# Kernel tuning notes

Measured on AMD Instinct MI355X. Metric: run time of the kernel, lower is better.

The kernel has to match this reference:

```python
import jax, jax.numpy as jnp
from jax import lax
import numpy as np

VOCAB = 50000
EMBED = 300
H = 128
NUM_CLASS = 2
B, L = 4, 512


def _lstm(x, Wih, Whh, b):
    # x: (B, L, D) -> hidden sequence (B, L, H); PyTorch gate order i,f,g,o
    Bn = x.shape[0]
    h0 = jnp.zeros((Bn, H), dtype=x.dtype)
    c0 = jnp.zeros((Bn, H), dtype=x.dtype)

    def step(carry, xt):
        h, c = carry
        g = xt @ Wih + h @ Whh + b  # (B, 4H)
        i, f, gg, o = jnp.split(g, 4, axis=-1)
        i = jax.nn.sigmoid(i)
        f = jax.nn.sigmoid(f)
        gg = jnp.tanh(gg)
        o = jax.nn.sigmoid(o)
        c = f * c + i * gg
        h = o * jnp.tanh(c)
        return (h, c), h

    _, hs = lax.scan(step, (h0, c0), jnp.swapaxes(x, 0, 1))
    return jnp.swapaxes(hs, 0, 1)


def setup_inputs() -> dict:
    key = jax.random.key(0)
    ks = jax.random.split(key, 12)
    s = lambda fan_in: 1.0 / np.sqrt(fan_in)
    inp = {
        "question_content": jax.random.randint(ks[0], (B, L), 0, VOCAB, dtype=jnp.int32),
        "answer_content": jax.random.randint(ks[1], (B, L), 0, VOCAB, dtype=jnp.int32),
        "embed_table": jax.random.normal(ks[2], (VOCAB, EMBED), dtype=jnp.float32) * 0.1,
        "W_ih": jax.random.uniform(ks[3], (EMBED, 4 * H), jnp.float32, -s(H), s(H)),
        "W_hh": jax.random.uniform(ks[4], (H, 4 * H), jnp.float32, -s(H), s(H)),
        "b_lstm": jax.random.uniform(ks[5], (4 * H,), jnp.float32, -s(H), s(H)),
        "Wa": jax.random.uniform(ks[6], (2 * H, H), jnp.float32, -s(2 * H), s(2 * H)),
        "ba": jnp.zeros((H,), jnp.float32),
        "Wq": jax.random.uniform(ks[7], (2 * H, 1), jnp.float32, -s(2 * H), s(2 * H)),
        "bq": jnp.zeros((1,), jnp.float32),
        "Wans": jax.random.uniform(ks[8], (2 * H, 1), jnp.float32, -s(2 * H), s(2 * H)),
        "bans": jnp.zeros((1,), jnp.float32),
        "Wlast": jax.random.uniform(ks[9], (2 * H, NUM_CLASS), jnp.float32, -s(2 * H), s(2 * H)),
        "blast": jnp.zeros((NUM_CLASS,), jnp.float32),
    }
    return inp


def reference(question_content, answer_content, embed_table, W_ih, W_hh, b_lstm,
              Wa, ba, Wq, bq, Wans, bans, Wlast, blast):
    q_emb = embed_table[question_content]  # (B, Lq, EMBED)
    a_emb = embed_table[answer_content]    # (B, La, EMBED)
    q_lstm = _lstm(q_emb, W_ih, W_hh, b_lstm)  # (B, Lq, H)
    a_lstm = _lstm(a_emb, W_ih, W_hh, b_lstm)  # (B, La, H)

    # A = tanh(Wa @ cat(q_expand, a_expand) + ba); split Wa to avoid the concat copy
    Wa_q, Wa_a = Wa[:H], Wa[H:]
    proj_q = q_lstm @ Wa_q              # (B, Lq, H)
    proj_a = a_lstm @ Wa_a              # (B, La, H)
    A = jnp.tanh(proj_q[:, :, None, :] + proj_a[:, None, :, :] + ba)  # (B, Lq, La, H)

    r_q = jnp.max(A, axis=1)  # max over question positions -> (B, La, H)
    r_a = jnp.max(A, axis=2)  # max over answer positions   -> (B, Lq, H)

    cat_q = jnp.concatenate([q_lstm, r_q], axis=-1)  # (B, L, 2H) (Lq == La)
    cat_a = jnp.concatenate([a_lstm, r_a], axis=-1)
    alpha_q = jax.nn.softmax(cat_q @ Wq + bq, axis=-2)    # (B, L, 1)
    alpha_a = jax.nn.softmax(cat_a @ Wans + bans, axis=-2)

    feature_q = jnp.sum(alpha_q * r_q, axis=-2)  # (B, H)
    feature_a = jnp.sum(alpha_a * r_a, axis=-2)  # (B, H)
    feature_last = jnp.concatenate([feature_q, feature_a], axis=-1)  # (B, 2H)

    score = jax.nn.log_softmax(feature_last @ Wlast + blast, axis=-1)
    predict = jnp.argmax(score, axis=-1)
    return score, predict
```

## Files before the change

kernel.cpp:

```cpp
#include <hip/hip_runtime.h>
#include <hip/hip_bf16.h>

#define EMBED 300
#define HD    128
#define LLEN  512
#define G4    512

#define OFF_LSTM 2097152
#define OFF_PROJ 2621440
#define OFF_MX   3145728

typedef _Float16 half8 __attribute__((ext_vector_type(8)));
typedef float    f32x4 __attribute__((ext_vector_type(4)));

__device__ __forceinline__ float fsig(float x) {
    return __fdividef(1.f, 1.f + __expf(-x));
}
__device__ __forceinline__ float ftanh(float x) {
    return 1.f - __fdividef(2.f, __expf(2.f * x) + 1.f);
}

__global__ __launch_bounds__(256) void k1_gemm(
    const int* __restrict__ qc, const int* __restrict__ ac,
    const float* __restrict__ emb, const float* __restrict__ wih,
    const float* __restrict__ bl, float* __restrict__ preg)
{
    __shared__ float As[32][65];
    __shared__ float Bs[32][64];
    const int m0 = blockIdx.x * 64;
    const int n0 = blockIdx.y * 64;
    const int tid = threadIdx.x;
    const int tx = tid & 15, ty = tid >> 4;
    float acc[4][4] = {};

    for (int k0 = 0; k0 < 300; k0 += 32) {
        #pragma unroll
        for (int i = 0; i < 8; ++i) {
            int e = tid + i * 256;
            int m = e >> 5, kk = e & 31;
            int row = m0 + m;
            int c = row >> 11, b = (row >> 9) & 3, t = row & 511;
            int tok = (c == 0 ? qc : ac)[b * LLEN + t];
            int k = k0 + kk;
            As[kk][m] = (k < 300) ? emb[(size_t)tok * EMBED + k] : 0.f;
        }
        #pragma unroll
        for (int i = 0; i < 8; ++i) {
            int e = tid + i * 256;
            int kk = e >> 6, n = e & 63;
            int k = k0 + kk;
            Bs[kk][n] = (k < 300) ? wih[k * G4 + n0 + n] : 0.f;
        }
        __syncthreads();
        #pragma unroll
        for (int kk = 0; kk < 32; ++kk) {
            float a[4], bv[4];
            #pragma unroll
            for (int i = 0; i < 4; ++i) a[i] = As[kk][ty * 4 + i];
            #pragma unroll
            for (int j = 0; j < 4; ++j) bv[j] = Bs[kk][tx * 4 + j];
            #pragma unroll
            for (int i = 0; i < 4; ++i)
                #pragma unroll
                for (int j = 0; j < 4; ++j)
                    acc[i][j] += a[i] * bv[j];
        }
        __syncthreads();
    }
    #pragma unroll
    for (int i = 0; i < 4; ++i) {
        int row = m0 + ty * 4 + i;
        #pragma unroll
        for (int j = 0; j < 4; ++j) {
            int n = n0 + tx * 4 + j;
            preg[(size_t)row * G4 + n] = acc[i][j] + bl[n];
        }
    }
}

__global__ __launch_bounds__(512, 1) void k2_lstm_mfma(
    const float* __restrict__ whh, const float* __restrict__ preg,
    const float* __restrict__ wa,
    float* __restrict__ lstm, float* __restrict__ proj, float* __restrict__ mx)
{
    const int seq = blockIdx.x;
    const int tid = threadIdx.x;
    const int w  = tid >> 6;
    const int l  = tid & 63;
    const int li = l & 15;
    const int g  = l >> 4;

    __shared__ __align__(16) _Float16 h0[128];
    __shared__ __align__(16) _Float16 h1[128];

    half8 afrag[4][4];
    #pragma unroll
    for (int s = 0; s < 4; ++s) {
        const int mg = s * 128 + w * 16 + li;
        #pragma unroll
        for (int kt = 0; kt < 4; ++kt) {
            half8 v;
            #pragma unroll
            for (int e = 0; e < 8; ++e)
                v[e] = (_Float16)whh[(kt * 32 + g * 8 + e) * G4 + mg];
            afrag[kt][s] = v;
        }
    }
    const int s_side = seq >> 2;
    half8 afragW[4];
    #pragma unroll
    for (int kt = 0; kt < 4; ++kt) {
        half8 v;
        #pragma unroll
        for (int e = 0; e < 8; ++e)
            v[e] = (_Float16)wa[(s_side * 128 + kt * 32 + g * 8 + e) * 128 + (w * 16 + li)];
        afragW[kt] = v;
    }

    if (tid < 128) { h0[tid] = (_Float16)0.f; h1[tid] = (_Float16)0.f; }

    const f32x4* pg4 = (const f32x4*)(preg + (size_t)seq * LLEN * G4);
    const int pgo = w * 4 + g;
    const int r   = li & 3;
    const int unit = w * 16 + g * 4 + r;
    const bool wlane = li < 4;
    float* outp = lstm + (size_t)seq * LLEN * HD + unit;
    float* prp  = proj + (size_t)seq * LLEN * HD + unit;
    float cst = 0.f;
    float pm = -1e30f;

    f32x4 pgA[4], pgB[4];
    #pragma unroll
    for (int s = 0; s < 4; ++s) pgA[s] = pg4[0 * 128 + s * 32 + pgo];
    #pragma unroll
    for (int s = 0; s < 4; ++s) pgB[s] = pg4[1 * 128 + s * 32 + pgo];

    __syncthreads();

#define LSTM_STEP(T, PGV, RD, WR)                                              \
    {                                                                          \
        half8 bfrag[4];                                                        \
        _Pragma("unroll")                                                      \
        for (int kt = 0; kt < 4; ++kt)                                         \
            bfrag[kt] = *(const half8*)((RD) + kt * 32 + g * 8);               \
        f32x4 a0 = PGV[0], a1 = PGV[1], a2 = PGV[2], a3 = PGV[3];              \
        {                                                                      \
            int tp = (T) + 2; if (tp > 511) tp = 511;                          \
            _Pragma("unroll")                                                  \
            for (int s = 0; s < 4; ++s) PGV[s] = pg4[tp * 128 + s * 32 + pgo]; \
        }                                                                      \
        _Pragma("unroll")                                                      \
        for (int kt = 0; kt < 4; ++kt) {                                       \
            a0 = __builtin_amdgcn_mfma_f32_16x16x32_f16(afrag[kt][0], bfrag[kt], a0, 0, 0, 0); \
            a1 = __builtin_amdgcn_mfma_f32_16x16x32_f16(afrag[kt][1], bfrag[kt], a1, 0, 0, 0); \
            a2 = __builtin_amdgcn_mfma_f32_16x16x32_f16(afrag[kt][2], bfrag[kt], a2, 0, 0, 0); \
            a3 = __builtin_amdgcn_mfma_f32_16x16x32_f16(afrag[kt][3], bfrag[kt], a3, 0, 0, 0); \
        }                                                                      \
        f32x4 ap = {0.f, 0.f, 0.f, 0.f};                                       \
        _Pragma("unroll")                                                      \
        for (int kt = 0; kt < 4; ++kt)                                         \
            ap = __builtin_amdgcn_mfma_f32_16x16x32_f16(afragW[kt], bfrag[kt], ap, 0, 0, 0); \
        float xi = (r == 0) ? a0[0] : (r == 1) ? a0[1] : (r == 2) ? a0[2] : a0[3]; \
        float xf = (r == 0) ? a1[0] : (r == 1) ? a1[1] : (r == 2) ? a1[2] : a1[3]; \
        float xg = (r == 0) ? a2[0] : (r == 1) ? a2[1] : (r == 2) ? a2[2] : a2[3]; \
        float xo = (r == 0) ? a3[0] : (r == 1) ? a3[1] : (r == 2) ? a3[2] : a3[3]; \
        float ps = (r == 0) ? ap[0] : (r == 1) ? ap[1] : (r == 2) ? ap[2] : ap[3]; \
        pm = fmaxf(pm, ps);                                                    \
        float i_ = fsig(xi), f_ = fsig(xf), g_ = ftanh(xg), o_ = fsig(xo);     \
        cst = f_ * cst + i_ * g_;                                              \
        float h = o_ * ftanh(cst);                                             \
        if (wlane) {                                                           \
            outp[(size_t)(T) * HD] = h;                                        \
            if ((T) > 0) prp[(size_t)((T) - 1) * HD] = ps;                     \
            (WR)[unit] = (_Float16)h;                                          \
        }                                                                      \
        asm volatile("s_waitcnt lgkmcnt(0)" ::: "memory");                     \
        __builtin_amdgcn_sched_barrier(0);                                     \
        __builtin_amdgcn_s_barrier();                                          \
        __builtin_amdgcn_sched_barrier(0);                                     \
    }

    #pragma unroll 1
    for (int tt = 0; tt < 256; ++tt) {
        const int t0 = tt * 2;
        LSTM_STEP(t0,     pgA, h0, h1);
        LSTM_STEP(t0 + 1, pgB, h1, h0);
    }
#undef LSTM_STEP

    {
        half8 bfin[4];
        #pragma unroll
        for (int kt = 0; kt < 4; ++kt)
            bfin[kt] = *(const half8*)(h0 + kt * 32 + g * 8);
        f32x4 ap = {0.f, 0.f, 0.f, 0.f};
        #pragma unroll
        for (int kt = 0; kt < 4; ++kt)
            ap = __builtin_amdgcn_mfma_f32_16x16x32_f16(afragW[kt], bfin[kt], ap, 0, 0, 0);
        float ps = (r == 0) ? ap[0] : (r == 1) ? ap[1] : (r == 2) ? ap[2] : ap[3];
        pm = fmaxf(pm, ps);
        if (wlane) {
            prp[(size_t)511 * HD] = ps;
            mx[seq * HD + unit] = pm;
        }
    }
}

__global__ __launch_bounds__(512) void k45_attn(
    const float* __restrict__ lstm, const float* __restrict__ proj,
    const float* __restrict__ mx, const float* __restrict__ ba,
    const float* __restrict__ wq, const float* __restrict__ wans,
    const float* __restrict__ wlast, const float* __restrict__ blast,
    float* __restrict__ outp)
{
    const int b = blockIdx.x;
    const int tid = threadIdx.x;
    const int wave = tid >> 6, lane = tid & 63;
    const int s = wave >> 2;
    const int ws = wave & 3;

    __shared__ float nred[8][128];
    __shared__ float dred[8];
    __shared__ float feats[2][128];
    __shared__ float cls[256];

    const float* wv = (s == 0) ? wq : wans;
    const float* lb = lstm + ((size_t)(s * 4 + b)) * LLEN * HD;
    const float* po = proj + ((size_t)((1 - s) * 4 + b)) * LLEN * HD;

    const float mb1 = mx[(s * 4 + b) * HD + lane] + ba[lane];
    const float mb2 = mx[(s * 4 + b) * HD + lane + 64] + ba[lane + 64];
    const float wv1a = wv[lane], wv1b = wv[lane + 64];
    const float wv2a = wv[128 + lane], wv2b = wv[192 + lane];

    float n1 = 0.f, n2 = 0.f, den = 0.f;
    #pragma unroll 4
    for (int jj = 0; jj < 128; ++jj) {
        const int j = ws + jj * 4;
        float L1 = lb[(size_t)j * HD + lane];
        float L2 = lb[(size_t)j * HD + lane + 64];
        float P1 = po[(size_t)j * HD + lane];
        float P2 = po[(size_t)j * HD + lane + 64];
        float r1 = ftanh(mb1 + P1), r2 = ftanh(mb2 + P2);
        float sc = L1 * wv1a + L2 * wv1b + r1 * wv2a + r2 * wv2b;
        #pragma unroll
        for (int o = 32; o; o >>= 1) sc += __shfl_xor(sc, o, 64);
        float e = __expf(sc);
        den += e;
        n1 += e * r1;
        n2 += e * r2;
    }
    nred[wave][lane] = n1;
    nred[wave][lane + 64] = n2;
    if (lane == 0) dred[wave] = den;
    __syncthreads();

    if (tid < 256) {
        const int ss = tid >> 7, h = tid & 127;
        float num = nred[ss * 4 + 0][h] + nred[ss * 4 + 1][h]
                  + nred[ss * 4 + 2][h] + nred[ss * 4 + 3][h];
        float dd  = dred[ss * 4 + 0] + dred[ss * 4 + 1]
                  + dred[ss * 4 + 2] + dred[ss * 4 + 3];
        feats[ss][h] = num / dd;
    }
    __syncthreads();

    if (tid < 128) {
        float f0 = feats[0][tid], f1 = feats[1][tid];
        cls[tid]       = f0 * wlast[tid * 2 + 0] + f1 * wlast[(128 + tid) * 2 + 0];
        cls[128 + tid] = f0 * wlast[tid * 2 + 1] + f1 * wlast[(128 + tid) * 2 + 1];
    }
    __syncthreads();
    if (tid < 64) {
        float a0 = cls[tid] + cls[tid + 64];
        float a1 = cls[128 + tid] + cls[192 + tid];
        #pragma unroll
        for (int o = 32; o; o >>= 1) {
            a0 += __shfl_down(a0, o, 64);
            a1 += __shfl_down(a1, o, 64);
        }
        if (tid == 0) {
            float l0 = blast[0] + a0, l1 = blast[1] + a1;
            float mxl = fmaxf(l0, l1);
            float lse = mxl + logf(__expf(l0 - mxl) + __expf(l1 - mxl));
            outp[b * 2 + 0] = l0 - lse;
            outp[b * 2 + 1] = l1 - lse;
            outp[8 + b]     = (l1 > l0) ? 1.f : 0.f;
        }
    }
}

extern "C" void kernel_launch(void* const* d_in, const int* in_sizes, int n_in,
                              void* d_out, int out_size, void* d_ws, size_t ws_size,
                              hipStream_t stream)
{
    const int*   qc    = (const int*)d_in[0];
    const int*   ac    = (const int*)d_in[1];
    const float* emb   = (const float*)d_in[2];
    const float* wih   = (const float*)d_in[3];
    const float* whh   = (const float*)d_in[4];
    const float* bl    = (const float*)d_in[5];
    const float* wa    = (const float*)d_in[6];
    const float* ba    = (const float*)d_in[7];
    const float* wq    = (const float*)d_in[8];
    const float* wans  = (const float*)d_in[10];
    const float* wlast = (const float*)d_in[12];
    const float* blast = (const float*)d_in[13];

    float* ws   = (float*)d_ws;
    float* preg = ws;
    float* lstm = ws + OFF_LSTM;
    float* proj = ws + OFF_PROJ;
    float* mx   = ws + OFF_MX;

    k1_gemm<<<dim3(64, 8), 256, 0, stream>>>(qc, ac, emb, wih, bl, preg);
    k2_lstm_mfma<<<8, 512, 0, stream>>>(whh, preg, wa, lstm, proj, mx);
    k45_attn<<<4, 512, 0, stream>>>(lstm, proj, mx, ba, wq, wans,
                                    wlast, blast, (float*)d_out);
}
```

Measured before the change: 438.2 us.

## Batch Wa projection over 16-step hidden history and split attention across more blocks

The LSTM kernel now keeps a 32-slot ring of fp16 hidden states in shared memory. Every 16 steps it computes the Wa projection for those 16 timesteps with one set of MFMAs, instead of running 4 extra MFMAs and scattered stores on every serial step. This takes work off the latency-bound recurrence critical path. The attention kernel is split into 32 blocks that each produce partial numerators and denominators, and a small final kernel reduces them, which raises parallelism in exchange for an extra launch.

```diff
diff --git a/kernel.cpp b/kernel.cpp
--- a/kernel.cpp
+++ b/kernel.cpp
@@ -90,8 +90,7 @@
     const int li = l & 15;
     const int g  = l >> 4;
 
-    __shared__ __align__(16) _Float16 h0[128];
-    __shared__ __align__(16) _Float16 h1[128];
+    __shared__ __align__(16) _Float16 hist[32 * 136];
 
     half8 afrag[4][4];
     #pragma unroll
@@ -117,7 +116,7 @@
         afragW[kt] = v;
     }
 
-    if (tid < 128) { h0[tid] = (_Float16)0.f; h1[tid] = (_Float16)0.f; }
+    for (int i = tid; i < 32 * 68; i += 512) ((unsigned*)hist)[i] = 0u;
 
     const f32x4* pg4 = (const f32x4*)(preg + (size_t)seq * LLEN * G4);
     const int pgo = w * 4 + g;
@@ -125,9 +124,8 @@
     const int unit = w * 16 + g * 4 + r;
     const bool wlane = li < 4;
     float* outp = lstm + (size_t)seq * LLEN * HD + unit;
-    float* prp  = proj + (size_t)seq * LLEN * HD + unit;
     float cst = 0.f;
-    float pm = -1e30f;
+    float pmr0 = -1e30f, pmr1 = -1e30f, pmr2 = -1e30f, pmr3 = -1e30f;
 
     f32x4 pgA[4], pgB[4];
     #pragma unroll
@@ -156,22 +154,15 @@
             a2 = __builtin_amdgcn_mfma_f32_16x16x32_f16(afrag[kt][2], bfrag[kt], a2, 0, 0, 0); \
             a3 = __builtin_amdgcn_mfma_f32_16x16x32_f16(afrag[kt][3], bfrag[kt], a3, 0, 0, 0); \
         }                                                                      \
-        f32x4 ap = {0.f, 0.f, 0.f, 0.f};                                       \
-        _Pragma("unroll")                                                      \
-        for (int kt = 0; kt < 4; ++kt)                                         \
-            ap = __builtin_amdgcn_mfma_f32_16x16x32_f16(afragW[kt], bfrag[kt], ap, 0, 0, 0); \
         float xi = (r == 0) ? a0[0] : (r == 1) ? a0[1] : (r == 2) ? a0[2] : a0[3]; \
         float xf = (r == 0) ? a1[0] : (r == 1) ? a1[1] : (r == 2) ? a1[2] : a1[3]; \
         float xg = (r == 0) ? a2[0] : (r == 1) ? a2[1] : (r == 2) ? a2[2] : a2[3]; \
         float xo = (r == 0) ? a3[0] : (r == 1) ? a3[1] : (r == 2) ? a3[2] : a3[3]; \
-        float ps = (r == 0) ? ap[0] : (r == 1) ? ap[1] : (r == 2) ? ap[2] : ap[3]; \
-        pm = fmaxf(pm, ps);                                                    \
         float i_ = fsig(xi), f_ = fsig(xf), g_ = ftanh(xg), o_ = fsig(xo);     \
         cst = f_ * cst + i_ * g_;                                              \
         float h = o_ * ftanh(cst);                                             \
         if (wlane) {                                                           \
             outp[(size_t)(T) * HD] = h;                                        \
-            if ((T) > 0) prp[(size_t)((T) - 1) * HD] = ps;                     \
             (WR)[unit] = (_Float16)h;                                          \
         }                                                                      \
         asm volatile("s_waitcnt lgkmcnt(0)" ::: "memory");                     \
@@ -183,60 +174,79 @@
     #pragma unroll 1
     for (int tt = 0; tt < 256; ++tt) {
         const int t0 = tt * 2;
-        LSTM_STEP(t0,     pgA, h0, h1);
-        LSTM_STEP(t0 + 1, pgB, h1, h0);
+        const int slot = t0 & 31;
+        _Float16* wr0 = hist + slot * 136;
+        const _Float16* rd0 = hist + ((slot + 31) & 31) * 136;
+        _Float16* wr1 = hist + (slot + 1) * 136;
+        LSTM_STEP(t0,     pgA, rd0, wr0);
+        LSTM_STEP(t0 + 1, pgB, wr0, wr1);
+        if ((tt & 7) == 7) {
+            const int p = (tt >> 3) & 1;
+            const int tbase = t0 - 14;
+            const _Float16* hb = hist + (p * 16 + li) * 136;
+            half8 bb0 = *(const half8*)(hb + 0 * 32 + g * 8);
+            half8 bb1 = *(const half8*)(hb + 1 * 32 + g * 8);
+            half8 bb2 = *(const half8*)(hb + 2 * 32 + g * 8);
+            half8 bb3 = *(const half8*)(hb + 3 * 32 + g * 8);
+            f32x4 pa = {0.f, 0.f, 0.f, 0.f};
+            pa = __builtin_amdgcn_mfma_f32_16x16x32_f16(afragW[0], bb0, pa, 0, 0, 0);
+            pa = __builtin_amdgcn_mfma_f32_16x16x32_f16(afragW[1], bb1, pa, 0, 0, 0);
+            pa = __builtin_amdgcn_mfma_f32_16x16x32_f16(afragW[2], bb2, pa, 0, 0, 0);
+            pa = __builtin_amdgcn_mfma_f32_16x16x32_f16(afragW[3], bb3, pa, 0, 0, 0);
+            float* pp = proj + (size_t)seq * LLEN * HD
+                      + (size_t)(tbase + li) * HD + w * 16 + g * 4;
+            *(f32x4*)pp = pa;
+            pmr0 = fmaxf(pmr0, pa[0]);
+            pmr1 = fmaxf(pmr1, pa[1]);
+            pmr2 = fmaxf(pmr2, pa[2]);
+            pmr3 = fmaxf(pmr3, pa[3]);
+        }
     }
 #undef LSTM_STEP
 
-    {
-        half8 bfin[4];
-        #pragma unroll
-        for (int kt = 0; kt < 4; ++kt)
-            bfin[kt] = *(const half8*)(h0 + kt * 32 + g * 8);
-        f32x4 ap = {0.f, 0.f, 0.f, 0.f};
-        #pragma unroll
-        for (int kt = 0; kt < 4; ++kt)
-            ap = __builtin_amdgcn_mfma_f32_16x16x32_f16(afragW[kt], bfin[kt], ap, 0, 0, 0);
-        float ps = (r == 0) ? ap[0] : (r == 1) ? ap[1] : (r == 2) ? ap[2] : ap[3];
-        pm = fmaxf(pm, ps);
-        if (wlane) {
-            prp[(size_t)511 * HD] = ps;
-            mx[seq * HD + unit] = pm;
-        }
-    }
-}
-
-__global__ __launch_bounds__(512) void k45_attn(
+    #pragma unroll
+    for (int m = 1; m <= 8; m <<= 1) {
+        pmr0 = fmaxf(pmr0, __shfl_xor(pmr0, m, 64));
+        pmr1 = fmaxf(pmr1, __shfl_xor(pmr1, m, 64));
+        pmr2 = fmaxf(pmr2, __shfl_xor(pmr2, m, 64));
+        pmr3 = fmaxf(pmr3, __shfl_xor(pmr3, m, 64));
+    }
+    if (li == 0) {
+        mx[seq * HD + w * 16 + g * 4 + 0] = pmr0;
+        mx[seq * HD + w * 16 + g * 4 + 1] = pmr1;
+        mx[seq * HD + w * 16 + g * 4 + 2] = pmr2;
+        mx[seq * HD + w * 16 + g * 4 + 3] = pmr3;
+    }
+}
+
+__global__ __launch_bounds__(512) void k45a_attn(
     const float* __restrict__ lstm, const float* __restrict__ proj,
     const float* __restrict__ mx, const float* __restrict__ ba,
     const float* __restrict__ wq, const float* __restrict__ wans,
-    const float* __restrict__ wlast, const float* __restrict__ blast,
-    float* __restrict__ outp)
-{
-    const int b = blockIdx.x;
+    float* __restrict__ pn, float* __restrict__ pd)
+{
+    const int bid = blockIdx.x;
+    const int chunk = bid & 3, sb = bid >> 2;
+    const int s = sb >> 2, b = sb & 3;
     const int tid = threadIdx.x;
     const int wave = tid >> 6, lane = tid & 63;
-    const int s = wave >> 2;
-    const int ws = wave & 3;
 
     __shared__ float nred[8][128];
     __shared__ float dred[8];
-    __shared__ float feats[2][128];
-    __shared__ float cls[256];
 
     const float* wv = (s == 0) ? wq : wans;
-    const float* lb = lstm + ((size_t)(s * 4 + b)) * LLEN * HD;
-    const float* po = proj + ((size_t)((1 - s) * 4 + b)) * LLEN * HD;
-
-    const float mb1 = mx[(s * 4 + b) * HD + lane] + ba[lane];
-    const float mb2 = mx[(s * 4 + b) * HD + lane + 64] + ba[lane + 64];
+    const float* lb = lstm + (size_t)sb * LLEN * HD;
+    const float* po = proj + (size_t)((1 - s) * 4 + b) * LLEN * HD;
+
+    const float mb1 = mx[sb * HD + lane] + ba[lane];
+    const float mb2 = mx[sb * HD + lane + 64] + ba[lane + 64];
     const float wv1a = wv[lane], wv1b = wv[lane + 64];
     const float wv2a = wv[128 + lane], wv2b = wv[192 + lane];
 
     float n1 = 0.f, n2 = 0.f, den = 0.f;
     #pragma unroll 4
-    for (int jj = 0; jj < 128; ++jj) {
-        const int j = ws + jj * 4;
+    for (int jj = 0; jj < 16; ++jj) {
+        const int j = chunk * 128 + wave + jj * 8;
         float L1 = lb[(size_t)j * HD + lane];
         float L2 = lb[(size_t)j * HD + lane + 64];
         float P1 = po[(size_t)j * HD + lane];
@@ -255,12 +265,36 @@
     if (lane == 0) dred[wave] = den;
     __syncthreads();
 
-    if (tid < 256) {
+    if (tid < 128) {
+        float s8 = 0.f;
+        #pragma unroll
+        for (int i = 0; i < 8; ++i) s8 += nred[i][tid];
+        pn[bid * 128 + tid] = s8;
+    }
+    if (tid == 128) {
+        float dd = 0.f;
+        #pragma unroll
+        for (int i = 0; i < 8; ++i) dd += dred[i];
+        pd[bid] = dd;
+    }
+}
+
+__global__ __launch_bounds__(256) void k45b_final(
+    const float* __restrict__ pn, const float* __restrict__ pd,
+    const float* __restrict__ wlast, const float* __restrict__ blast,
+    float* __restrict__ outp)
+{
+    const int b = blockIdx.x;
+    const int tid = threadIdx.x;
+    __shared__ float feats[2][128];
+    __shared__ float cls[256];
+
+    {
         const int ss = tid >> 7, h = tid & 127;
-        float num = nred[ss * 4 + 0][h] + nred[ss * 4 + 1][h]
-                  + nred[ss * 4 + 2][h] + nred[ss * 4 + 3][h];
-        float dd  = dred[ss * 4 + 0] + dred[ss * 4 + 1]
-                  + dred[ss * 4 + 2] + dred[ss * 4 + 3];
+        const int base = (ss * 4 + b) * 4;
+        float num = pn[(base + 0) * 128 + h] + pn[(base + 1) * 128 + h]
+                  + pn[(base + 2) * 128 + h] + pn[(base + 3) * 128 + h];
+        float dd  = pd[base + 0] + pd[base + 1] + pd[base + 2] + pd[base + 3];
         feats[ss][h] = num / dd;
     }
     __syncthreads();
@@ -312,9 +346,11 @@
     float* lstm = ws + OFF_LSTM;
     float* proj = ws + OFF_PROJ;
     float* mx   = ws + OFF_MX;
+    float* pn   = ws;
+    float* pd   = ws + 4096;
 
     k1_gemm<<<dim3(64, 8), 256, 0, stream>>>(qc, ac, emb, wih, bl, preg);
     k2_lstm_mfma<<<8, 512, 0, stream>>>(whh, preg, wa, lstm, proj, mx);
-    k45_attn<<<4, 512, 0, stream>>>(lstm, proj, mx, ba, wq, wans,
-                                    wlast, blast, (float*)d_out);
-}
+    k45a_attn<<<32, 512, 0, stream>>>(lstm, proj, mx, ba, wq, wans, pn, pd);
+    k45b_final<<<4, 256, 0, stream>>>(pn, pd, wlast, blast, (float*)d_out);
+}
```

Result: faster. 389.9 us (-11.0%).
